# Kernel tuning notes

Hardware: AMD Instinct MI355X
Metric: run time of the kernel (lower is better)

## Reference

```python
import jax, jax.numpy as jnp
import numpy as np

EPS = 1e-12

def _l2norm(v):
    return v / (jnp.linalg.norm(v) + EPS)

def _spectral_norm_weight(W, u):
    # torch spectral_norm with n_power_iterations=1: v = norm(W^T u); u' = norm(W v);
    # sigma = u'^T W v with u', v detached; returns W / sigma.
    v = jax.lax.stop_gradient(_l2norm(W.T @ u))
    u2 = jax.lax.stop_gradient(_l2norm(W @ v))
    sigma = u2 @ (W @ v)
    return W / sigma

def setup_inputs() -> dict:
    key = jax.random.key(0)
    ks = jax.random.split(key, 8)
    C, H, W = 64, 96, 96
    Cfg = C // 8
    g = 1e-2  # small weight scale (module uses orthogonal init with tiny gain)
    return {
        "x":  jax.random.normal(ks[0], (1, C, H, W), jnp.float32),
        "Wf": jax.random.normal(ks[1], (Cfg, C), jnp.float32) * g,
        "bf": jnp.zeros((Cfg,), jnp.float32),
        "Wg": jax.random.normal(ks[2], (Cfg, C), jnp.float32) * g,
        "bg": jnp.zeros((Cfg,), jnp.float32),
        "Wh": jax.random.normal(ks[3], (C, C), jnp.float32) * g,
        "bh": jnp.zeros((C,), jnp.float32),
        "gamma": jax.random.normal(ks[4], (1,), jnp.float32),
        "uf": jax.random.normal(ks[5], (Cfg,), jnp.float32),
        "ug": jax.random.normal(ks[6], (Cfg,), jnp.float32),
        "uh": jax.random.normal(ks[7], (C,), jnp.float32),
    }

def reference(x, Wf, bf, Wg, bg, Wh, bh, gamma, uf, ug, uh):
    B, C, H, Wd = x.shape
    N = H * Wd
    xf = x.reshape(B, C, N)  # 1x1 convs act per-pixel -> matmul over channel dim
    Wf_sn = _spectral_norm_weight(Wf, uf)
    Wg_sn = _spectral_norm_weight(Wg, ug)
    Wh_sn = _spectral_norm_weight(Wh, uh)
    f_flat = jnp.einsum('oc,bcn->bon', Wf_sn, xf) + bf[:, None]  # [B,Cfg,N]
    g_flat = jnp.einsum('oc,bcn->bon', Wg_sn, xf) + bg[:, None]  # [B,Cfg,N]
    h_flat = jnp.einsum('oc,bcn->bon', Wh_sn, xf) + bh[:, None]  # [B,C,N]
    # s[b,n,m] = sum_k g[b,k,n] * f[b,k,m]  (g^T f)
    s = jnp.einsum('bkn,bkm->bnm', g_flat, f_flat)  # [B,N,N]
    beta = jax.nn.softmax(s, axis=1)                # softmax over dim=1 (g axis)
    o = jnp.einsum('bcn,bnm->bcm', h_flat, beta)    # [B,C,N]
    o = o.reshape(B, C, H, Wd)
    return gamma * o + x
```

## Files before the change

kernel.cpp:

```cpp
#include <hip/hip_runtime.h>
#include <hip/hip_bf16.h>

#define NPIX 9216
#define MTILES (NPIX / 16)

typedef __attribute__((ext_vector_type(4))) float f32x4;
typedef __attribute__((ext_vector_type(8))) short bf16x8;
typedef __attribute__((ext_vector_type(2))) unsigned int u32x2;

__device__ __forceinline__ void gload_lds16(const void* g, void* l) {
  __builtin_amdgcn_global_load_lds(
      (const __attribute__((address_space(1))) unsigned int*)g,
      (__attribute__((address_space(3))) unsigned int*)l, 16, 0, 0);
}
__device__ __forceinline__ void gload_lds4(const void* g, void* l) {
  __builtin_amdgcn_global_load_lds(
      (const __attribute__((address_space(1))) unsigned int*)g,
      (__attribute__((address_space(3))) unsigned int*)l, 4, 0, 0);
}
#define LDS_OFF(p) ((unsigned)(unsigned long long)(const __attribute__((address_space(3))) char*)(const char*)(p))

__global__ __launch_bounds__(256) void fgh_kernel(
    const float* __restrict__ x,
    const float* __restrict__ Wf, const float* __restrict__ bfv,
    const float* __restrict__ Wg, const float* __restrict__ bgv,
    const float* __restrict__ Wh, const float* __restrict__ bhv,
    const float* __restrict__ uf, const float* __restrict__ ug,
    const float* __restrict__ uh,
    ushort* __restrict__ Qp, ushort* __restrict__ Kp, ushort* __restrict__ Vt2) {
  __shared__ float vsh3[3][64];
  __shared__ float is_s[3];
  const int tid = threadIdx.x;
  const int wv = tid >> 6, t = tid & 63;
  if (wv < 3) {
    const float* W = (wv == 0) ? Wf : (wv == 1) ? Wg : Wh;
    const float* u = (wv == 0) ? uf : (wv == 1) ? ug : uh;
    const int O = (wv == 2) ? 64 : 8;
    float v = 0.f;
    for (int o = 0; o < O; ++o) v += W[o * 64 + t] * u[o];
    float s = v * v;
    for (int off = 32; off; off >>= 1) s += __shfl_xor(s, off);
    vsh3[wv][t] = v / (sqrtf(s) + 1e-12f);
    float wvv = 0.f;
    if (t < O) { for (int c = 0; c < 64; ++c) wvv += W[t * 64 + c] * vsh3[wv][c]; }
    float s2 = (t < O) ? wvv * wvv : 0.f;
    for (int off = 32; off; off >>= 1) s2 += __shfl_xor(s2, off);
    const float nw = sqrtf(s2);
    if (t == 0) is_s[wv] = (nw + 1e-12f) / s2;
  }
  __syncthreads();

  const float LOG2E = 1.44269504f;
  const int px = tid & 63;
  const int rw = __builtin_amdgcn_readfirstlane(tid >> 6);
  const int r0 = blockIdx.y * 16 + rw * 4;
  const int p  = blockIdx.x * 64 + px;

  float xv[64];
  #pragma unroll
  for (int c = 0; c < 64; ++c) xv[c] = x[c * NPIX + p];

  const float* W0;
  float scl;
  if (r0 < 8)       { W0 = Wf + r0 * 64;        scl = is_s[0]; }
  else if (r0 < 16) { W0 = Wg + (r0 - 8) * 64;  scl = is_s[1]; }
  else              { W0 = Wh + (r0 - 16) * 64; scl = is_s[2]; }

  float acc[4] = {0.f, 0.f, 0.f, 0.f};
  #pragma unroll
  for (int c = 0; c < 64; ++c) {
    const float xc = xv[c];
    acc[0] += W0[c]       * xc;
    acc[1] += W0[64 + c]  * xc;
    acc[2] += W0[128 + c] * xc;
    acc[3] += W0[192 + c] * xc;
  }

  const int tile = p >> 5, nt = p & 31;
  const int tt = nt >> 4, gg = (nt >> 2) & 3, ii = nt & 3;
  const int kbase = tile * 512 + nt * 8;
  #pragma unroll
  for (int j = 0; j < 4; ++j) {
    const int r = r0 + j;
    if (r < 8) {
      const float val = (acc[j] * scl + bfv[r]) * 0.25f * LOG2E;
      const __hip_bfloat16 h = __float2bfloat16(val);
      Qp[p * 16 + r] = *(const ushort*)&h;
    } else if (r < 16) {
      const int rk = r - 8;
      const float val = acc[j] * scl + bgv[rk];
      const __hip_bfloat16 h = __float2bfloat16(val);
      Kp[kbase + rk] = *(const ushort*)&h;
    } else {
      const int rv = r - 16;
      const float val = acc[j] * scl + bhv[rv];
      const __hip_bfloat16 hv = __float2bfloat16(val);
      const int idx = tile * 2048 +
          ((rv * 32 + gg * 8 + tt * 4 + ii) ^ (((rv >> 1) & 7) << 3));
      Vt2[idx] = *(const ushort*)&hv;
    }
  }
}

template <int S>
__global__ __launch_bounds__(256) void attn_kernel(
    const ushort* __restrict__ Qp, const ushort* __restrict__ Kp,
    const ushort* __restrict__ Vt2,
    ushort* __restrict__ Om,
    float* __restrict__ Sm) {
  constexpr int NSEG = NPIX / S;
  constexpr int NT = NSEG / 32;
  __shared__ ushort Vs[4][2048];
  __shared__ ushort Ks[4][512];
  const int tid  = threadIdx.x;
  const int w    = tid >> 6;
  const int l    = tid & 63;
  const int mloc = l & 15;
  const int g    = l >> 4;
  const int spl  = blockIdx.y;
  const int mrow = blockIdx.x * 64 + w * 16 + mloc;

  bf16x8 qh = *(const bf16x8*)(Qp + mrow * 16);
  asm volatile("" : "+v"(qh));

  const int n0 = spl * NSEG;
  const char* vsrc = (const char*)Vt2 + ((size_t)(n0 >> 5)) * 4096 + w * 1024 + l * 16;
  const char* ksrc = (const char*)Kp + ((size_t)(n0 >> 5)) * 1024 + w * 256 + l * 4;

  #define STAGE(t_) do {                                                  \
    const int b_ = (t_) & 3;                                              \
    gload_lds16(vsrc + (size_t)(t_) * 4096, (char*)&Vs[b_][0] + w * 1024);\
    gload_lds4 (ksrc + (size_t)(t_) * 1024, (char*)&Ks[b_][0] + w * 256); \
  } while (0)

  STAGE(0);
  STAGE(1);

  const unsigned ks_base = LDS_OFF(&Ks[0][0]);
  const unsigned vs_base = LDS_OFF(&Vs[0][0]);
  const unsigned vswz = (mloc * 64 + g * 16) ^ (((mloc >> 1) & 7) << 4);

  float ls = 0.f;
  const f32x4 zero = {0.f, 0.f, 0.f, 0.f};
  f32x4 acc0 = zero, acc1 = zero, acc2 = zero, acc3 = zero;

  for (int t = 0; t < NT; ++t) {
    const int b = t & 3;
    if (t + 2 < NT) {
      STAGE(t + 2);
      asm volatile("s_waitcnt vmcnt(4)" ::: "memory");
    } else if (t + 1 < NT) {
      asm volatile("s_waitcnt vmcnt(2)" ::: "memory");
    } else {
      asm volatile("s_waitcnt vmcnt(0)" ::: "memory");
    }
    __builtin_amdgcn_s_barrier();

    const unsigned kaddr = ks_base + b * 1024 + mloc * 16;
    const unsigned vaddr = vs_base + b * 4096 + vswz;
    bf16x8 kh0, kh1, v0, v1, v2, v3;
    asm volatile("ds_read_b128 %0, %1"            : "=v"(kh0) : "v"(kaddr));
    asm volatile("ds_read_b128 %0, %1 offset:256" : "=v"(kh1) : "v"(kaddr));
    asm volatile("ds_read_b128 %0, %1"            : "=v"(v0)  : "v"(vaddr));
    asm volatile("ds_read_b128 %0, %1 offset:1024": "=v"(v1)  : "v"(vaddr));
    asm volatile("ds_read_b128 %0, %1 offset:2048": "=v"(v2)  : "v"(vaddr));
    asm volatile("ds_read_b128 %0, %1 offset:3072": "=v"(v3)  : "v"(vaddr));
    asm volatile("s_waitcnt lgkmcnt(4)" ::: "memory");
    __builtin_amdgcn_sched_barrier(0);

    f32x4 s0 = zero, s1 = zero;
    s0 = __builtin_amdgcn_mfma_f32_16x16x32_bf16(kh0, qh, s0, 0, 0, 0);
    s1 = __builtin_amdgcn_mfma_f32_16x16x32_bf16(kh1, qh, s1, 0, 0, 0);

    float pj[8];
    pj[0] = exp2f(s0[0] - 16.f); pj[1] = exp2f(s0[1] - 16.f);
    pj[2] = exp2f(s0[2] - 16.f); pj[3] = exp2f(s0[3] - 16.f);
    pj[4] = exp2f(s1[0] - 16.f); pj[5] = exp2f(s1[1] - 16.f);
    pj[6] = exp2f(s1[2] - 16.f); pj[7] = exp2f(s1[3] - 16.f);
    ls += ((pj[0] + pj[1]) + (pj[2] + pj[3])) + ((pj[4] + pj[5]) + (pj[6] + pj[7]));

    union { unsigned int u[4]; bf16x8 v; } pu;
    #pragma unroll
    for (int jj = 0; jj < 4; ++jj) {
      unsigned int r;
      asm("v_cvt_pk_bf16_f32 %0, %1, %2" : "=v"(r) : "v"(pj[2 * jj]), "v"(pj[2 * jj + 1]));
      pu.u[jj] = r;
    }
    asm volatile("s_waitcnt lgkmcnt(0)" ::: "memory");
    __builtin_amdgcn_sched_barrier(0);
    acc0 = __builtin_amdgcn_mfma_f32_16x16x32_bf16(pu.v, v0, acc0, 0, 0, 0);
    acc1 = __builtin_amdgcn_mfma_f32_16x16x32_bf16(pu.v, v1, acc1, 0, 0, 0);
    acc2 = __builtin_amdgcn_mfma_f32_16x16x32_bf16(pu.v, v2, acc2, 0, 0, 0);
    acc3 = __builtin_amdgcn_mfma_f32_16x16x32_bf16(pu.v, v3, acc3, 0, 0, 0);
  }
  #undef STAGE

  ls += __shfl_xor(ls, 16);
  ls += __shfl_xor(ls, 32);

  const size_t mt = (size_t)blockIdx.x * 4 + w;
  ushort* Ob = Om + (mt * S + spl) * 1024;
  float*  Sb = Sm + (mt * S + spl) * 32;
  #pragma unroll
  for (int ct = 0; ct < 4; ++ct) {
    const f32x4 a = (ct == 0) ? acc0 : (ct == 1) ? acc1 : (ct == 2) ? acc2 : acc3;
    unsigned int r0, r1;
    asm("v_cvt_pk_bf16_f32 %0, %1, %2" : "=v"(r0) : "v"(a[0]), "v"(a[1]));
    asm("v_cvt_pk_bf16_f32 %0, %1, %2" : "=v"(r1) : "v"(a[2]), "v"(a[3]));
    u32x2 pk; pk[0] = r0; pk[1] = r1;
    *(u32x2*)(Ob + (ct * 16 + mloc) * 16 + 4 * g) = pk;
  }
  if (l < 16) { Sb[16 + l] = ls; }
}

template <int S>
__global__ __launch_bounds__(256) void combine_kernel(
    const ushort* __restrict__ Om, const float* __restrict__ Sm,
    const float* __restrict__ x, const float* __restrict__ gammap,
    float* __restrict__ out) {
  const int mt = blockIdx.x >> 2;
  const int m0 = mt * 16;
  const int e  = (blockIdx.x & 3) * 256 + threadIdx.x;
  const float gamma = gammap[0];
  const float* Sb = Sm + (size_t)mt * S * 32;
  const ushort* Ob = Om + (size_t)mt * S * 1024;
  const int m = e & 15, c = e >> 4;
  float L = 0.f, val = 0.f;
  #pragma unroll
  for (int s = 0; s < S; ++s) {
    L += Sb[s * 32 + 16 + m];
    union { unsigned int i; float f; } cv;
    cv.i = ((unsigned int)Ob[s * 1024 + e]) << 16;
    val += cv.f;
  }
  const int idx = c * NPIX + m0 + m;
  out[idx] = gamma * (val / L) + x[idx];
}

extern "C" void kernel_launch(void* const* d_in, const int* in_sizes, int n_in,
                              void* d_out, int out_size, void* d_ws, size_t ws_size,
                              hipStream_t stream) {
  const float* x     = (const float*)d_in[0];
  const float* Wf    = (const float*)d_in[1];
  const float* bf    = (const float*)d_in[2];
  const float* Wg    = (const float*)d_in[3];
  const float* bg    = (const float*)d_in[4];
  const float* Wh    = (const float*)d_in[5];
  const float* bh    = (const float*)d_in[6];
  const float* gamma = (const float*)d_in[7];
  const float* uf    = (const float*)d_in[8];
  const float* ug    = (const float*)d_in[9];
  const float* uh    = (const float*)d_in[10];
  float* out = (float*)d_out;

  char* ws = (char*)d_ws;
  ushort* Qp  = (ushort*)(ws + 256);
  ushort* Kp  = (ushort*)(ws + 256 + NPIX * 16 * 2);
  ushort* Vt2 = (ushort*)(ws + 256 + 2 * NPIX * 16 * 2);
  const size_t off = 256 + (size_t)2 * NPIX * 16 * 2 + (size_t)NPIX * 64 * 2;
  ushort* Om = (ushort*)(ws + off);
  const size_t need16 = off + (size_t)MTILES * 16 * 1024 * 2 + (size_t)MTILES * 16 * 32 * 4;

  fgh_kernel<<<dim3(NPIX / 64, 5), 256, 0, stream>>>(x, Wf, bf, Wg, bg, Wh, bh,
                                                     uf, ug, uh, Qp, Kp, Vt2);
  if (ws_size >= need16) {
    float* Sm = (float*)(ws + off + (size_t)MTILES * 16 * 1024 * 2);
    attn_kernel<16><<<dim3(NPIX / 64, 16), 256, 0, stream>>>(Qp, Kp, Vt2, Om, Sm);
    combine_kernel<16><<<MTILES * 4, 256, 0, stream>>>(Om, Sm, x, gamma, out);
  } else {
    float* Sm = (float*)(ws + off + (size_t)MTILES * 8 * 1024 * 2);
    attn_kernel<8><<<dim3(NPIX / 64, 8), 256, 0, stream>>>(Qp, Kp, Vt2, Om, Sm);
    combine_kernel<8><<<MTILES * 4, 256, 0, stream>>>(Om, Sm, x, gamma, out);
  }
}
```

Measured before the change: 71.45 us.

## Switch attention MFMAs to 32x32x16 tiles with 128 rows per block

Replaces the 16x16x32 MFMAs in the attention kernel with 32x32x16 ones: one score MFMA per 32-key tile and four PV MFMAs into two 16-wide accumulators. Each block now covers 128 query rows, so each staged K/V tile is reused by twice as many rows. The V layout written by the projection kernel and the query scaling are rewritten to match the new operand layout, since the duplicated k-sum that needed the 0.25 factor is gone. The risks are higher register pressure from the 16-float accumulators and fewer blocks in the grid.

```diff
diff --git a/kernel.cpp b/kernel.cpp
--- a/kernel.cpp
+++ b/kernel.cpp
@@ -5,6 +5,7 @@
 #define MTILES (NPIX / 16)
 
 typedef __attribute__((ext_vector_type(4))) float f32x4;
+typedef __attribute__((ext_vector_type(16))) float f32x16;
 typedef __attribute__((ext_vector_type(8))) short bf16x8;
 typedef __attribute__((ext_vector_type(2))) unsigned int u32x2;
 
@@ -76,14 +77,15 @@
     acc[3] += W0[192 + c] * xc;
   }
 
-  const int tile = p >> 5, nt = p & 31;
-  const int tt = nt >> 4, gg = (nt >> 2) & 3, ii = nt & 3;
-  const int kbase = tile * 512 + nt * 8;
+  const int tile = p >> 5, nn = p & 31;
+  const int kbase = tile * 512 + nn * 8;
+  const int vfix = (nn >> 4) * 512 + ((nn >> 2) & 1) * 256
+                 + (nn & 3) + 4 * ((nn >> 3) & 1);
   #pragma unroll
   for (int j = 0; j < 4; ++j) {
     const int r = r0 + j;
     if (r < 8) {
-      const float val = (acc[j] * scl + bfv[r]) * 0.25f * LOG2E;
+      const float val = (acc[j] * scl + bfv[r]) * LOG2E;
       const __hip_bfloat16 h = __float2bfloat16(val);
       Qp[p * 16 + r] = *(const ushort*)&h;
     } else if (r < 16) {
@@ -95,9 +97,8 @@
       const int rv = r - 16;
       const float val = acc[j] * scl + bhv[rv];
       const __hip_bfloat16 hv = __float2bfloat16(val);
-      const int idx = tile * 2048 +
-          ((rv * 32 + gg * 8 + tt * 4 + ii) ^ (((rv >> 1) & 7) << 3));
-      Vt2[idx] = *(const ushort*)&hv;
+      const int vidx = tile * 2048 + (rv >> 5) * 1024 + vfix + (rv & 31) * 8;
+      Vt2[vidx] = *(const ushort*)&hv;
     }
   }
 }
@@ -115,12 +116,14 @@
   const int tid  = threadIdx.x;
   const int w    = tid >> 6;
   const int l    = tid & 63;
-  const int mloc = l & 15;
-  const int g    = l >> 4;
+  const int cc   = l & 31;
+  const int h    = l >> 5;
   const int spl  = blockIdx.y;
-  const int mrow = blockIdx.x * 64 + w * 16 + mloc;
+  const int mrow = blockIdx.x * 128 + w * 32 + cc;
 
   bf16x8 qh = *(const bf16x8*)(Qp + mrow * 16);
+  const bf16x8 zero8 = {0, 0, 0, 0, 0, 0, 0, 0};
+  if (l >= 32) qh = zero8;
   asm volatile("" : "+v"(qh));
 
   const int n0 = spl * NSEG;
@@ -138,11 +141,11 @@
 
   const unsigned ks_base = LDS_OFF(&Ks[0][0]);
   const unsigned vs_base = LDS_OFF(&Vs[0][0]);
-  const unsigned vswz = (mloc * 64 + g * 16) ^ (((mloc >> 1) & 7) << 4);
 
   float ls = 0.f;
-  const f32x4 zero = {0.f, 0.f, 0.f, 0.f};
-  f32x4 acc0 = zero, acc1 = zero, acc2 = zero, acc3 = zero;
+  const f32x16 zero16 = {0.f,0.f,0.f,0.f,0.f,0.f,0.f,0.f,
+                         0.f,0.f,0.f,0.f,0.f,0.f,0.f,0.f};
+  f32x16 accL = zero16, accH = zero16;
 
   for (int t = 0; t < NT; ++t) {
     const int b = t & 3;
@@ -156,61 +159,70 @@
     }
     __builtin_amdgcn_s_barrier();
 
-    const unsigned kaddr = ks_base + b * 1024 + mloc * 16;
-    const unsigned vaddr = vs_base + b * 4096 + vswz;
-    bf16x8 kh0, kh1, v0, v1, v2, v3;
-    asm volatile("ds_read_b128 %0, %1"            : "=v"(kh0) : "v"(kaddr));
-    asm volatile("ds_read_b128 %0, %1 offset:256" : "=v"(kh1) : "v"(kaddr));
-    asm volatile("ds_read_b128 %0, %1"            : "=v"(v0)  : "v"(vaddr));
-    asm volatile("ds_read_b128 %0, %1 offset:1024": "=v"(v1)  : "v"(vaddr));
-    asm volatile("ds_read_b128 %0, %1 offset:2048": "=v"(v2)  : "v"(vaddr));
-    asm volatile("ds_read_b128 %0, %1 offset:3072": "=v"(v3)  : "v"(vaddr));
+    const unsigned kaddr = ks_base + b * 1024 + cc * 16;
+    const unsigned vaddr = vs_base + b * 4096 + l * 16;
+    bf16x8 kf, v00, v01, v10, v11;
+    asm volatile("ds_read_b128 %0, %1"            : "=v"(kf)  : "v"(kaddr));
+    asm volatile("ds_read_b128 %0, %1"            : "=v"(v00) : "v"(vaddr));
+    asm volatile("ds_read_b128 %0, %1 offset:1024": "=v"(v01) : "v"(vaddr));
+    asm volatile("ds_read_b128 %0, %1 offset:2048": "=v"(v10) : "v"(vaddr));
+    asm volatile("ds_read_b128 %0, %1 offset:3072": "=v"(v11) : "v"(vaddr));
     asm volatile("s_waitcnt lgkmcnt(4)" ::: "memory");
     __builtin_amdgcn_sched_barrier(0);
 
-    f32x4 s0 = zero, s1 = zero;
-    s0 = __builtin_amdgcn_mfma_f32_16x16x32_bf16(kh0, qh, s0, 0, 0, 0);
-    s1 = __builtin_amdgcn_mfma_f32_16x16x32_bf16(kh1, qh, s1, 0, 0, 0);
-
-    float pj[8];
-    pj[0] = exp2f(s0[0] - 16.f); pj[1] = exp2f(s0[1] - 16.f);
-    pj[2] = exp2f(s0[2] - 16.f); pj[3] = exp2f(s0[3] - 16.f);
-    pj[4] = exp2f(s1[0] - 16.f); pj[5] = exp2f(s1[1] - 16.f);
-    pj[6] = exp2f(s1[2] - 16.f); pj[7] = exp2f(s1[3] - 16.f);
-    ls += ((pj[0] + pj[1]) + (pj[2] + pj[3])) + ((pj[4] + pj[5]) + (pj[6] + pj[7]));
-
-    union { unsigned int u[4]; bf16x8 v; } pu;
+    f32x16 s = zero16;
+    s = __builtin_amdgcn_mfma_f32_32x32x16_bf16(kf, qh, s, 0, 0, 0);
+
+    float pj[16];
+    #pragma unroll
+    for (int r = 0; r < 16; ++r) pj[r] = exp2f(s[r] - 16.f);
+    float lsum = 0.f;
+    #pragma unroll
+    for (int r = 0; r < 16; ++r) lsum += pj[r];
+    ls += lsum;
+
+    union { unsigned int u[4]; bf16x8 v; } pa0, pa1;
     #pragma unroll
     for (int jj = 0; jj < 4; ++jj) {
-      unsigned int r;
-      asm("v_cvt_pk_bf16_f32 %0, %1, %2" : "=v"(r) : "v"(pj[2 * jj]), "v"(pj[2 * jj + 1]));
-      pu.u[jj] = r;
-    }
+      unsigned int ra, rb;
+      asm("v_cvt_pk_bf16_f32 %0, %1, %2" : "=v"(ra) : "v"(pj[2 * jj]), "v"(pj[2 * jj + 1]));
+      asm("v_cvt_pk_bf16_f32 %0, %1, %2" : "=v"(rb) : "v"(pj[8 + 2 * jj]), "v"(pj[9 + 2 * jj]));
+      pa0.u[jj] = ra;
+      pa1.u[jj] = rb;
+    }
+
     asm volatile("s_waitcnt lgkmcnt(0)" ::: "memory");
     __builtin_amdgcn_sched_barrier(0);
-    acc0 = __builtin_amdgcn_mfma_f32_16x16x32_bf16(pu.v, v0, acc0, 0, 0, 0);
-    acc1 = __builtin_amdgcn_mfma_f32_16x16x32_bf16(pu.v, v1, acc1, 0, 0, 0);
-    acc2 = __builtin_amdgcn_mfma_f32_16x16x32_bf16(pu.v, v2, acc2, 0, 0, 0);
-    acc3 = __builtin_amdgcn_mfma_f32_16x16x32_bf16(pu.v, v3, acc3, 0, 0, 0);
+    accL = __builtin_amdgcn_mfma_f32_32x32x16_bf16(pa0.v, v00, accL, 0, 0, 0);
+    accL = __builtin_amdgcn_mfma_f32_32x32x16_bf16(pa1.v, v01, accL, 0, 0, 0);
+    accH = __builtin_amdgcn_mfma_f32_32x32x16_bf16(pa0.v, v10, accH, 0, 0, 0);
+    accH = __builtin_amdgcn_mfma_f32_32x32x16_bf16(pa1.v, v11, accH, 0, 0, 0);
   }
   #undef STAGE
 
-  ls += __shfl_xor(ls, 16);
   ls += __shfl_xor(ls, 32);
 
-  const size_t mt = (size_t)blockIdx.x * 4 + w;
-  ushort* Ob = Om + (mt * S + spl) * 1024;
-  float*  Sb = Sm + (mt * S + spl) * 32;
-  #pragma unroll
-  for (int ct = 0; ct < 4; ++ct) {
-    const f32x4 a = (ct == 0) ? acc0 : (ct == 1) ? acc1 : (ct == 2) ? acc2 : acc3;
-    unsigned int r0, r1;
-    asm("v_cvt_pk_bf16_f32 %0, %1, %2" : "=v"(r0) : "v"(a[0]), "v"(a[1]));
-    asm("v_cvt_pk_bf16_f32 %0, %1, %2" : "=v"(r1) : "v"(a[2]), "v"(a[3]));
-    u32x2 pk; pk[0] = r0; pk[1] = r1;
-    *(u32x2*)(Ob + (ct * 16 + mloc) * 16 + 4 * g) = pk;
-  }
-  if (l < 16) { Sb[16 + l] = ls; }
+  const size_t mt0 = (size_t)blockIdx.x * 8 + w * 2;
+  ushort* Ob0 = Om + (mt0 * S + spl) * 1024;
+  ushort* Ob1 = Om + ((mt0 + 1) * S + spl) * 1024;
+  float*  Sb0 = Sm + (mt0 * S + spl) * 32;
+  float*  Sb1 = Sm + ((mt0 + 1) * S + spl) * 32;
+  #pragma unroll
+  for (int ch = 0; ch < 2; ++ch) {
+    const f32x16 a = (ch == 0) ? accL : accH;
+    #pragma unroll
+    for (int r = 0; r < 16; r += 2) {
+      unsigned int pk;
+      asm("v_cvt_pk_bf16_f32 %0, %1, %2" : "=v"(pk) : "v"(a[r]), "v"(a[r + 1]));
+      const int m16 = (r & 3) + 8 * ((r >> 2) & 1) + 4 * h;
+      ushort* Ob = (r < 8) ? Ob0 : Ob1;
+      *(unsigned int*)(Ob + (ch * 32 + cc) * 16 + m16) = pk;
+    }
+  }
+  if (l < 32) {
+    float* SbX = (l < 16) ? Sb0 : Sb1;
+    SbX[16 + (l & 15)] = ls;
+  }
 }
 
 template <int S>
@@ -265,11 +277,11 @@
                                                      uf, ug, uh, Qp, Kp, Vt2);
   if (ws_size >= need16) {
     float* Sm = (float*)(ws + off + (size_t)MTILES * 16 * 1024 * 2);
-    attn_kernel<16><<<dim3(NPIX / 64, 16), 256, 0, stream>>>(Qp, Kp, Vt2, Om, Sm);
+    attn_kernel<16><<<dim3(NPIX / 128, 16), 256, 0, stream>>>(Qp, Kp, Vt2, Om, Sm);
     combine_kernel<16><<<MTILES * 4, 256, 0, stream>>>(Om, Sm, x, gamma, out);
   } else {
     float* Sm = (float*)(ws + off + (size_t)MTILES * 8 * 1024 * 2);
-    attn_kernel<8><<<dim3(NPIX / 64, 8), 256, 0, stream>>>(Qp, Kp, Vt2, Om, Sm);
+    attn_kernel<8><<<dim3(NPIX / 128, 8), 256, 0, stream>>>(Qp, Kp, Vt2, Om, Sm);
     combine_kernel<8><<<MTILES * 4, 256, 0, stream>>>(Om, Sm, x, gamma, out);
   }
 }
```

Result: no change. 72.02 us (median of 2 runs) (+0.8%).
